# Optimization experiments

Hardware: AMD Instinct MI355X
Metric: run time of the kernel (lower is better)

Reference implementation:

```python
import jax, jax.numpy as jnp
import numpy as np

B, N = 4, 1024
D_MODEL, N_HEADS, D_HEAD, D_COORD = 512, 8, 64, 2


def setup_inputs() -> dict:
    key = jax.random.key(0)
    ks = jax.random.split(key, 8)
    sd = 1.0 / np.sqrt(D_MODEL)
    return {
        "x": jax.random.normal(ks[0], (B, N, D_MODEL), dtype=jnp.float32),
        "positions": jax.random.uniform(ks[1], (N, D_COORD), dtype=jnp.float32) * 32.0,
        "W_Q": jax.random.normal(ks[2], (D_MODEL, N_HEADS * D_HEAD), dtype=jnp.float32) * sd,
        "W_K": jax.random.normal(ks[3], (D_MODEL, N_HEADS * D_HEAD), dtype=jnp.float32) * sd,
        "W_V": jax.random.normal(ks[4], (D_MODEL, N_HEADS * D_HEAD), dtype=jnp.float32) * sd,
        "W_O": jax.random.normal(ks[5], (N_HEADS * D_HEAD, D_MODEL), dtype=jnp.float32) * sd,
        "U": jax.random.normal(ks[6], (N_HEADS, D_HEAD, D_HEAD), dtype=jnp.float32),
        "freqs": jax.random.normal(ks[7], (N_HEADS, D_HEAD // 2, D_COORD), dtype=jnp.float32),
    }


def reference(x, positions, W_Q, W_K, W_V, W_O, U, freqs):
    # x: (B,N,d_model); positions: (N,d_coord); U: (H,dh,dh); freqs: (H,m,d_coord)
    Bn, Nn, _ = x.shape
    H, dh, _ = U.shape
    m = dh // 2
    scale = (dh // 2) ** -0.5

    Q = (x @ W_Q).reshape(Bn, Nn, H, dh)
    K = (x @ W_K).reshape(Bn, Nn, H, dh)
    V = (x @ W_V).reshape(Bn, Nn, H, dh)

    # Active-subspace projector: Pi = qr(U)[0] @ qr(U)[0].T per head
    Uq = jax.vmap(lambda u: jnp.linalg.qr(u)[0])(U)              # (H,dh,dh)
    P = jnp.einsum('hde,hfe->hdf', Uq, Uq)                       # U U^T
    Qp = jnp.einsum('bnhd,hdf->bhnf', Q, P)                      # (B,H,N,dh)
    Kp = jnp.einsum('bnhd,hdf->bhnf', K, P)

    # Relative rotation: R_rel(r_j - r_i) is block-diag 2x2 rotations with
    # angle theta_ijm = freqs_m . (r_j - r_i) = a_jm - a_im (separable), so
    # q^T R(r_j-r_i) k = (R(a_i)q)^T (R(a_j)k)  -- exact RoPE identity.
    ang = jnp.einsum('nc,hmc->hnm', positions, freqs)            # (H,N,m)
    c = jnp.cos(ang)[None]                                       # (1,H,N,m)
    s = jnp.sin(ang)[None]

    def rot(v):  # v: (B,H,N,dh) -> rotated (even, odd) halves (B,H,N,m)
        ve, vo = v[..., ::2], v[..., 1::2]
        return ve * c - vo * s, ve * s + vo * c

    qe, qo = rot(Qp)
    ke, ko = rot(Kp)
    scores = (jnp.einsum('bhim,bhjm->bhij', qe, ke)
              + jnp.einsum('bhim,bhjm->bhij', qo, ko)) * scale   # (B,H,N,N)
    w = jax.nn.softmax(scores, axis=-1)
    out = jnp.einsum('bhij,bjhd->bihd', w, V).reshape(Bn, Nn, H * dh)
    return out @ W_O
```

## Files before the change

### kernel.cpp

```cpp
#include <hip/hip_runtime.h>
#include <math.h>

#define NBATCH 4
#define NSEQ   1024
#define DMODEL 512
#define NH     8
#define DH     64
#define MROWS  (NBATCH*NSEQ)
#define MHALF  (DH/2)

typedef __attribute__((ext_vector_type(8))) short bf16x8;
typedef __attribute__((ext_vector_type(4))) float floatx4;

__device__ __forceinline__ ushort f2bf(float f) {
    union { float f; uint u; } v; v.f = f;
    uint r = v.u + 0x7fffu + ((v.u >> 16) & 1u);
    return (ushort)(r >> 16);
}

__global__ __launch_bounds__(256) void angles_kernel(
    const float* __restrict__ pos, const float* __restrict__ freqs,
    float* __restrict__ cosT, float* __restrict__ sinT)
{
    int idx = blockIdx.x * 256 + threadIdx.x;
    int m = idx & 31;
    int n = (idx >> 5) & 1023;
    int h = idx >> 15;
    float a = pos[n*2+0] * freqs[(h*MHALF+m)*2+0]
            + pos[n*2+1] * freqs[(h*MHALF+m)*2+1];
    cosT[idx] = cosf(a);
    sinT[idx] = sinf(a);
}

__global__ __launch_bounds__(256) void xprep_kernel(
    const float* __restrict__ x, ushort* __restrict__ xb)
{
    int idx = (blockIdx.x * 256 + threadIdx.x) * 8;
    float4 a = *(const float4*)&x[idx];
    float4 b = *(const float4*)&x[idx+4];
    uint4 pk;
    pk.x = (uint)f2bf(a.x) | ((uint)f2bf(a.y) << 16);
    pk.y = (uint)f2bf(a.z) | ((uint)f2bf(a.w) << 16);
    pk.z = (uint)f2bf(b.x) | ((uint)f2bf(b.y) << 16);
    pk.w = (uint)f2bf(b.z) | ((uint)f2bf(b.w) << 16);
    *(uint4*)&xb[idx] = pk;
}

__global__ __launch_bounds__(256) void wprep_kernel(
    const float* __restrict__ Wq, const float* __restrict__ Wk,
    const float* __restrict__ Wv, const float* __restrict__ Wo,
    ushort* __restrict__ Wt)
{
    __shared__ float T[64][65];
    int n0g = blockIdx.x * 64;
    int k0  = blockIdx.y * 64;
    int mat = n0g >> 9;
    const float* W = (mat == 0) ? Wq : ((mat == 1) ? Wk : ((mat == 2) ? Wv : Wo));
    int n0 = n0g & 511;
    int tid = threadIdx.x;
    int c = tid & 63, r = tid >> 6;
    #pragma unroll
    for (int i = 0; i < 16; i++)
        T[r + i*4][c] = W[(k0 + r + i*4) * DMODEL + n0 + c];
    __syncthreads();
    int nl = tid >> 2;
    int kg = tid & 3;
    #pragma unroll
    for (int g = 0; g < 4; g++) {
        int kl = kg * 16 + g * 4;
        uint2 pk;
        pk.x = (uint)f2bf(T[kl+0][nl]) | ((uint)f2bf(T[kl+1][nl]) << 16);
        pk.y = (uint)f2bf(T[kl+2][nl]) | ((uint)f2bf(T[kl+3][nl]) << 16);
        *(uint2*)&Wt[(size_t)(n0g + nl) * DMODEL + k0 + kl] = pk;
    }
}

__global__ __launch_bounds__(256) void qkv_gemm(
    const ushort* __restrict__ xb, const ushort* __restrict__ Wt,
    const float* __restrict__ cosT, const float* __restrict__ sinT,
    ushort* __restrict__ Qb, ushort* __restrict__ Kb, ushort* __restrict__ Vt)
{
    __shared__ ushort As[64 * 40];
    __shared__ ushort Bs[64 * 40];
    __shared__ float  Cs[64][65];

    const int cb = blockIdx.x;
    const int rb = blockIdx.y;
    const int mat = cb >> 3;
    const int c0 = (cb & 7) * 64;
    const int r0 = rb * 64;
    const int ng0 = mat * 512 + c0;

    const int tid = threadIdx.x;
    const int w = tid >> 6, l = tid & 63;
    const int lr = l & 15, lg = l >> 4;

    const int srow = tid >> 2;
    const int sgrp = tid & 3;

    floatx4 acc[4];
    #pragma unroll
    for (int nt = 0; nt < 4; nt++) acc[nt] = (floatx4){0.f,0.f,0.f,0.f};

    for (int k0 = 0; k0 < DMODEL; k0 += 32) {
        __syncthreads();
        *(uint4*)&As[srow*40 + sgrp*8] =
            *(const uint4*)&xb[(size_t)(r0 + srow) * DMODEL + k0 + sgrp*8];
        *(uint4*)&Bs[srow*40 + sgrp*8] =
            *(const uint4*)&Wt[(size_t)(ng0 + srow) * DMODEL + k0 + sgrp*8];
        __syncthreads();

        bf16x8 af = *(const bf16x8*)&As[(16*w + lr)*40 + lg*8];
        #pragma unroll
        for (int nt = 0; nt < 4; nt++) {
            bf16x8 bf = *(const bf16x8*)&Bs[(nt*16 + lr)*40 + lg*8];
            acc[nt] = __builtin_amdgcn_mfma_f32_16x16x32_bf16(af, bf, acc[nt], 0, 0, 0);
        }
    }

    __syncthreads();
    #pragma unroll
    for (int nt = 0; nt < 4; nt++)
        #pragma unroll
        for (int r = 0; r < 4; r++)
            Cs[16*w + lg*4 + r][nt*16 + lr] = acc[nt][r];
    __syncthreads();

    const int tx = tid & 15, ty = tid >> 4;
    const int dbase = (c0 + tx*4) & 63;
    const int h = (mat == 2) ? ((c0 + tx*4) >> 6) + 0 : 0;
    const int head = c0 >> 6;
    (void)h;

    if (mat == 2) {
        int rowbase = r0 + ty * 4;
        int b = rowbase >> 10, n0 = rowbase & 1023;
        size_t vbase = (size_t)(b * NH + head) * DH;
        #pragma unroll
        for (int j = 0; j < 4; j++) {
            ushort us[4];
            #pragma unroll
            for (int i = 0; i < 4; i++) us[i] = f2bf(Cs[ty*4 + i][tx*4 + j]);
            uint2 pk;
            pk.x = (uint)us[0] | ((uint)us[1] << 16);
            pk.y = (uint)us[2] | ((uint)us[3] << 16);
            *(uint2*)&Vt[(vbase + dbase + j) * NSEQ + n0] = pk;
        }
    } else {
        ushort* dst = (mat == 0) ? Qb : Kb;
        #pragma unroll
        for (int i = 0; i < 4; i++) {
            int row = r0 + ty * 4 + i;
            int b = row >> 10, n = row & 1023;
            float v[4];
            #pragma unroll
            for (int p = 0; p < 2; p++) {
                int de = dbase + 2 * p;
                int m = de >> 1;
                float c = cosT[(head * NSEQ + n) * MHALF + m];
                float s = sinT[(head * NSEQ + n) * MHALF + m];
                float ve = Cs[ty*4 + i][tx*4 + 2*p];
                float vo = Cs[ty*4 + i][tx*4 + 2*p + 1];
                v[2*p]     = ve * c - vo * s;
                v[2*p + 1] = ve * s + vo * c;
            }
            uint2 pk;
            pk.x = (uint)f2bf(v[0]) | ((uint)f2bf(v[1]) << 16);
            pk.y = (uint)f2bf(v[2]) | ((uint)f2bf(v[3]) << 16);
            *(uint2*)&dst[((size_t)(b * NH + head) * NSEQ + n) * DH + dbase] = pk;
        }
    }
}

__global__ __launch_bounds__(256) void attn_kernel(
    const ushort* __restrict__ Qb, const ushort* __restrict__ Kb,
    const ushort* __restrict__ Vt, ushort* __restrict__ Obb)
{
    __shared__ ushort Ks[64 * 72];
    __shared__ ushort Vs[64 * 72];
    __shared__ ushort Ps[64 * 72];

    const int tid = threadIdx.x;
    const int w = tid >> 6, l = tid & 63;
    const int lr = l & 15, lg = l >> 4;
    const int bh = blockIdx.y, q0 = blockIdx.x * 64;

    const ushort* Qg = Qb + (size_t)bh * NSEQ * DH;
    const ushort* Kg = Kb + (size_t)bh * NSEQ * DH;
    const ushort* Vg = Vt + (size_t)bh * DH * NSEQ;

    bf16x8 qf[2];
    #pragma unroll
    for (int ks = 0; ks < 2; ks++)
        qf[ks] = *(const bf16x8*)(Qg + (size_t)(q0 + 16*w + lr) * DH + ks*32 + lg*8);

    floatx4 ot[4];
    #pragma unroll
    for (int i = 0; i < 4; i++) ot[i] = (floatx4){0.f, 0.f, 0.f, 0.f};
    float m_run = -INFINITY, l_run = 0.f;
    const float scale = 0.17677669529663687f;

    const int sr = tid >> 2;
    const int sc = (tid & 3) * 16;

    for (int jt = 0; jt < 16; jt++) {
        __syncthreads();
        {
            const ushort* kp = Kg + (size_t)(jt*64 + sr) * DH + sc;
            uint4 ka = *(const uint4*)kp;
            uint4 kb = *(const uint4*)(kp + 8);
            *(uint4*)&Ks[sr*72 + sc]     = ka;
            *(uint4*)&Ks[sr*72 + sc + 8] = kb;
            const ushort* vp = Vg + (size_t)sr * NSEQ + jt*64 + sc;
            uint4 va = *(const uint4*)vp;
            uint4 vb = *(const uint4*)(vp + 8);
            *(uint4*)&Vs[sr*72 + sc]     = va;
            *(uint4*)&Vs[sr*72 + sc + 8] = vb;
        }
        __syncthreads();

        floatx4 st[4];
        #pragma unroll
        for (int jm = 0; jm < 4; jm++) {
            floatx4 acc = (floatx4){0.f, 0.f, 0.f, 0.f};
            #pragma unroll
            for (int ks = 0; ks < 2; ks++) {
                bf16x8 af = *(const bf16x8*)&Ks[(jm*16 + lr)*72 + ks*32 + lg*8];
                acc = __builtin_amdgcn_mfma_f32_16x16x32_bf16(af, qf[ks], acc, 0, 0, 0);
            }
            st[jm] = acc;
        }

        float mx = -INFINITY;
        #pragma unroll
        for (int jm = 0; jm < 4; jm++)
            #pragma unroll
            for (int r = 0; r < 4; r++) {
                st[jm][r] *= scale;
                mx = fmaxf(mx, st[jm][r]);
            }
        mx = fmaxf(mx, __shfl_xor(mx, 16, 64));
        mx = fmaxf(mx, __shfl_xor(mx, 32, 64));
        float mnew = fmaxf(m_run, mx);
        float alpha = __expf(m_run - mnew);
        m_run = mnew;

        float rsum = 0.f;
        #pragma unroll
        for (int jm = 0; jm < 4; jm++) {
            ushort us[4];
            #pragma unroll
            for (int r = 0; r < 4; r++) {
                float p = __expf(st[jm][r] - mnew);
                rsum += p;
                us[r] = f2bf(p);
            }
            uint2 pk;
            pk.x = (uint)us[0] | ((uint)us[1] << 16);
            pk.y = (uint)us[2] | ((uint)us[3] << 16);
            *(uint2*)&Ps[(16*w + lr)*72 + jm*16 + lg*4] = pk;
        }
        rsum += __shfl_xor(rsum, 16, 64);
        rsum += __shfl_xor(rsum, 32, 64);
        l_run = l_run * alpha + rsum;

        #pragma unroll
        for (int dt = 0; dt < 4; dt++)
            #pragma unroll
            for (int r = 0; r < 4; r++)
                ot[dt][r] *= alpha;

        bf16x8 pf[2];
        #pragma unroll
        for (int ks = 0; ks < 2; ks++)
            pf[ks] = *(const bf16x8*)&Ps[(16*w + lr)*72 + ks*32 + lg*8];
        #pragma unroll
        for (int dt = 0; dt < 4; dt++)
            #pragma unroll
            for (int ks = 0; ks < 2; ks++) {
                bf16x8 af = *(const bf16x8*)&Vs[(dt*16 + lr)*72 + ks*32 + lg*8];
                ot[dt] = __builtin_amdgcn_mfma_f32_16x16x32_bf16(af, pf[ks], ot[dt], 0, 0, 0);
            }
    }

    float inv = 1.f / l_run;
    int n = q0 + 16*w + lr;
    #pragma unroll
    for (int dt = 0; dt < 4; dt++) {
        uint2 pk;
        pk.x = (uint)f2bf(ot[dt][0] * inv) | ((uint)f2bf(ot[dt][1] * inv) << 16);
        pk.y = (uint)f2bf(ot[dt][2] * inv) | ((uint)f2bf(ot[dt][3] * inv) << 16);
        *(uint2*)&Obb[((size_t)bh * NSEQ + n) * DH + dt*16 + lg*4] = pk;
    }
}

__global__ __launch_bounds__(256) void out_gemm(
    const ushort* __restrict__ Obb, const ushort* __restrict__ Wt,
    float* __restrict__ out)
{
    __shared__ ushort As[64 * 40];
    __shared__ ushort Bs[64 * 40];
    __shared__ float  Cs[64][65];

    const int cb = blockIdx.x;
    const int rb = blockIdx.y;
    const int c0 = cb * 64, r0 = rb * 64;

    const int tid = threadIdx.x;
    const int w = tid >> 6, l = tid & 63;
    const int lr = l & 15, lg = l >> 4;
    const int srow = tid >> 2;
    const int sgrp = tid & 3;

    const int arow = r0 + srow;
    const int b = arow >> 10, n = arow & 1023;

    floatx4 acc[4];
    #pragma unroll
    for (int nt = 0; nt < 4; nt++) acc[nt] = (floatx4){0.f,0.f,0.f,0.f};

    for (int k0 = 0; k0 < DMODEL; k0 += 32) {
        int h = k0 >> 6;
        int d0 = k0 & 63;
        __syncthreads();
        *(uint4*)&As[srow*40 + sgrp*8] =
            *(const uint4*)&Obb[((size_t)(b * NH + h) * NSEQ + n) * DH + d0 + sgrp*8];
        *(uint4*)&Bs[srow*40 + sgrp*8] =
            *(const uint4*)&Wt[(size_t)(1536 + c0 + srow) * DMODEL + k0 + sgrp*8];
        __syncthreads();

        bf16x8 af = *(const bf16x8*)&As[(16*w + lr)*40 + lg*8];
        #pragma unroll
        for (int nt = 0; nt < 4; nt++) {
            bf16x8 bf = *(const bf16x8*)&Bs[(nt*16 + lr)*40 + lg*8];
            acc[nt] = __builtin_amdgcn_mfma_f32_16x16x32_bf16(af, bf, acc[nt], 0, 0, 0);
        }
    }

    __syncthreads();
    #pragma unroll
    for (int nt = 0; nt < 4; nt++)
        #pragma unroll
        for (int r = 0; r < 4; r++)
            Cs[16*w + lg*4 + r][nt*16 + lr] = acc[nt][r];
    __syncthreads();

    const int tx = tid & 15, ty = tid >> 4;
    #pragma unroll
    for (int i = 0; i < 4; i++) {
        float4 o;
        o.x = Cs[ty*4 + i][tx*4 + 0];
        o.y = Cs[ty*4 + i][tx*4 + 1];
        o.z = Cs[ty*4 + i][tx*4 + 2];
        o.w = Cs[ty*4 + i][tx*4 + 3];
        *(float4*)&out[(size_t)(r0 + ty*4 + i) * DMODEL + c0 + tx*4] = o;
    }
}

extern "C" void kernel_launch(void* const* d_in, const int* in_sizes, int n_in,
                              void* d_out, int out_size, void* d_ws, size_t ws_size,
                              hipStream_t stream) {
    const float* x         = (const float*)d_in[0];
    const float* positions = (const float*)d_in[1];
    const float* Wq        = (const float*)d_in[2];
    const float* Wk        = (const float*)d_in[3];
    const float* Wv        = (const float*)d_in[4];
    const float* Wo        = (const float*)d_in[5];
    const float* freqs     = (const float*)d_in[7];
    float* out = (float*)d_out;

    float*  ws   = (float*)d_ws;
    float*  cosT = ws;
    float*  sinT = cosT + NH*NSEQ*MHALF;
    ushort* xb   = (ushort*)(sinT + NH*NSEQ*MHALF);
    ushort* Wt   = xb + (size_t)MROWS*DMODEL;
    ushort* Qb   = Wt + (size_t)2048*DMODEL;
    ushort* Kb   = Qb + (size_t)NBATCH*NH*NSEQ*DH;
    ushort* Vt   = Kb + (size_t)NBATCH*NH*NSEQ*DH;
    ushort* Obb  = Vt + (size_t)NBATCH*NH*NSEQ*DH;

    angles_kernel<<<dim3(NH*NSEQ*MHALF/256), 256, 0, stream>>>(positions, freqs, cosT, sinT);
    xprep_kernel<<<dim3(MROWS*DMODEL/(256*8)), 256, 0, stream>>>(x, xb);
    wprep_kernel<<<dim3(32, 8), 256, 0, stream>>>(Wq, Wk, Wv, Wo, Wt);
    qkv_gemm<<<dim3(24, 64), 256, 0, stream>>>(xb, Wt, cosT, sinT, Qb, Kb, Vt);
    attn_kernel<<<dim3(16, 32), 256, 0, stream>>>(Qb, Kb, Vt, Obb);
    out_gemm<<<dim3(8, 64), 256, 0, stream>>>(Obb, Wt, out);
}
```

Measured before the change: 139.6 us.

## Split attention over key halves, prefetch K/V tiles, merge prep kernels

Attention now splits the key dimension into two halves (split-K flash attention) so twice as many blocks run, and writes fp32 partial outputs plus running max/sum that a new combine kernel merges. The K/V tile loads are register-prefetched one tile ahead to overlap global loads with MFMA work, and attention gets a launch-bounds occupancy hint. The three prep kernels are fused into one launch to cut launch overhead. In exchange it adds fp32 partial-output traffic and an extra kernel launch for the combine step.

New measurement: 130.7 us. -6.4%, faster.

```diff
diff --git a/kernel.cpp b/kernel.cpp
--- a/kernel.cpp
+++ b/kernel.cpp
@@ -18,60 +18,59 @@
     return (ushort)(r >> 16);
 }
 
-__global__ __launch_bounds__(256) void angles_kernel(
+__global__ __launch_bounds__(256) void prep_kernel(
     const float* __restrict__ pos, const float* __restrict__ freqs,
-    float* __restrict__ cosT, float* __restrict__ sinT)
-{
-    int idx = blockIdx.x * 256 + threadIdx.x;
-    int m = idx & 31;
-    int n = (idx >> 5) & 1023;
-    int h = idx >> 15;
-    float a = pos[n*2+0] * freqs[(h*MHALF+m)*2+0]
-            + pos[n*2+1] * freqs[(h*MHALF+m)*2+1];
-    cosT[idx] = cosf(a);
-    sinT[idx] = sinf(a);
-}
-
-__global__ __launch_bounds__(256) void xprep_kernel(
-    const float* __restrict__ x, ushort* __restrict__ xb)
-{
-    int idx = (blockIdx.x * 256 + threadIdx.x) * 8;
-    float4 a = *(const float4*)&x[idx];
-    float4 b = *(const float4*)&x[idx+4];
-    uint4 pk;
-    pk.x = (uint)f2bf(a.x) | ((uint)f2bf(a.y) << 16);
-    pk.y = (uint)f2bf(a.z) | ((uint)f2bf(a.w) << 16);
-    pk.z = (uint)f2bf(b.x) | ((uint)f2bf(b.y) << 16);
-    pk.w = (uint)f2bf(b.z) | ((uint)f2bf(b.w) << 16);
-    *(uint4*)&xb[idx] = pk;
-}
-
-__global__ __launch_bounds__(256) void wprep_kernel(
+    const float* __restrict__ x,
     const float* __restrict__ Wq, const float* __restrict__ Wk,
     const float* __restrict__ Wv, const float* __restrict__ Wo,
-    ushort* __restrict__ Wt)
+    float* __restrict__ cosT, float* __restrict__ sinT,
+    ushort* __restrict__ xb, ushort* __restrict__ Wt)
 {
     __shared__ float T[64][65];
-    int n0g = blockIdx.x * 64;
-    int k0  = blockIdx.y * 64;
-    int mat = n0g >> 9;
-    const float* W = (mat == 0) ? Wq : ((mat == 1) ? Wk : ((mat == 2) ? Wv : Wo));
-    int n0 = n0g & 511;
-    int tid = threadIdx.x;
-    int c = tid & 63, r = tid >> 6;
-    #pragma unroll
-    for (int i = 0; i < 16; i++)
-        T[r + i*4][c] = W[(k0 + r + i*4) * DMODEL + n0 + c];
-    __syncthreads();
-    int nl = tid >> 2;
-    int kg = tid & 3;
-    #pragma unroll
-    for (int g = 0; g < 4; g++) {
-        int kl = kg * 16 + g * 4;
-        uint2 pk;
-        pk.x = (uint)f2bf(T[kl+0][nl]) | ((uint)f2bf(T[kl+1][nl]) << 16);
-        pk.y = (uint)f2bf(T[kl+2][nl]) | ((uint)f2bf(T[kl+3][nl]) << 16);
-        *(uint2*)&Wt[(size_t)(n0g + nl) * DMODEL + k0 + kl] = pk;
+    const int bid = blockIdx.x;
+    const int tid = threadIdx.x;
+
+    if (bid < 1024) {
+        int idx = bid * 256 + tid;
+        int m = idx & 31;
+        int n = (idx >> 5) & 1023;
+        int h = idx >> 15;
+        float a = pos[n*2+0] * freqs[(h*MHALF+m)*2+0]
+                + pos[n*2+1] * freqs[(h*MHALF+m)*2+1];
+        cosT[idx] = cosf(a);
+        sinT[idx] = sinf(a);
+    } else if (bid < 2048) {
+        int idx = ((bid - 1024) * 256 + tid) * 8;
+        float4 a = *(const float4*)&x[idx];
+        float4 b = *(const float4*)&x[idx+4];
+        uint4 pk;
+        pk.x = (uint)f2bf(a.x) | ((uint)f2bf(a.y) << 16);
+        pk.y = (uint)f2bf(a.z) | ((uint)f2bf(a.w) << 16);
+        pk.z = (uint)f2bf(b.x) | ((uint)f2bf(b.y) << 16);
+        pk.w = (uint)f2bf(b.z) | ((uint)f2bf(b.w) << 16);
+        *(uint4*)&xb[idx] = pk;
+    } else {
+        int b2 = bid - 2048;
+        int n0g = (b2 & 31) * 64;
+        int k0  = (b2 >> 5) * 64;
+        int mat = n0g >> 9;
+        const float* W = (mat == 0) ? Wq : ((mat == 1) ? Wk : ((mat == 2) ? Wv : Wo));
+        int n0 = n0g & 511;
+        int c = tid & 63, r = tid >> 6;
+        #pragma unroll
+        for (int i = 0; i < 16; i++)
+            T[r + i*4][c] = W[(k0 + r + i*4) * DMODEL + n0 + c];
+        __syncthreads();
+        int nl = tid >> 2;
+        int kg = tid & 3;
+        #pragma unroll
+        for (int g = 0; g < 4; g++) {
+            int kl = kg * 16 + g * 4;
+            uint2 pk;
+            pk.x = (uint)f2bf(T[kl+0][nl]) | ((uint)f2bf(T[kl+1][nl]) << 16);
+            pk.y = (uint)f2bf(T[kl+2][nl]) | ((uint)f2bf(T[kl+3][nl]) << 16);
+            *(uint2*)&Wt[(size_t)(n0g + nl) * DMODEL + k0 + kl] = pk;
+        }
     }
 }
 
@@ -127,10 +126,8 @@
     __syncthreads();
 
     const int tx = tid & 15, ty = tid >> 4;
-    const int dbase = (c0 + tx*4) & 63;
-    const int h = (mat == 2) ? ((c0 + tx*4) >> 6) + 0 : 0;
+    const int dbase = tx * 4;
     const int head = c0 >> 6;
-    (void)h;
 
     if (mat == 2) {
         int rowbase = r0 + ty * 4;
@@ -172,9 +169,10 @@
     }
 }
 
-__global__ __launch_bounds__(256) void attn_kernel(
+__global__ __launch_bounds__(256, 4) void attn_kernel(
     const ushort* __restrict__ Qb, const ushort* __restrict__ Kb,
-    const ushort* __restrict__ Vt, ushort* __restrict__ Obb)
+    const ushort* __restrict__ Vt, float* __restrict__ Opart,
+    float2* __restrict__ Ml)
 {
     __shared__ ushort Ks[64 * 72];
     __shared__ ushort Vs[64 * 72];
@@ -184,6 +182,7 @@
     const int w = tid >> 6, l = tid & 63;
     const int lr = l & 15, lg = l >> 4;
     const int bh = blockIdx.y, q0 = blockIdx.x * 64;
+    const int z = blockIdx.z, jt0 = z * 8;
 
     const ushort* Qg = Qb + (size_t)bh * NSEQ * DH;
     const ushort* Kg = Kb + (size_t)bh * NSEQ * DH;
@@ -203,21 +202,29 @@
     const int sr = tid >> 2;
     const int sc = (tid & 3) * 16;
 
-    for (int jt = 0; jt < 16; jt++) {
-        __syncthreads();
-        {
-            const ushort* kp = Kg + (size_t)(jt*64 + sr) * DH + sc;
-            uint4 ka = *(const uint4*)kp;
-            uint4 kb = *(const uint4*)(kp + 8);
-            *(uint4*)&Ks[sr*72 + sc]     = ka;
-            *(uint4*)&Ks[sr*72 + sc + 8] = kb;
-            const ushort* vp = Vg + (size_t)sr * NSEQ + jt*64 + sc;
-            uint4 va = *(const uint4*)vp;
-            uint4 vb = *(const uint4*)(vp + 8);
-            *(uint4*)&Vs[sr*72 + sc]     = va;
-            *(uint4*)&Vs[sr*72 + sc + 8] = vb;
-        }
-        __syncthreads();
+    const ushort* kp = Kg + (size_t)(jt0*64 + sr) * DH + sc;
+    uint4 ka  = *(const uint4*)kp;
+    uint4 kb2 = *(const uint4*)(kp + 8);
+    const ushort* vp = Vg + (size_t)sr * NSEQ + jt0*64 + sc;
+    uint4 va  = *(const uint4*)vp;
+    uint4 vb2 = *(const uint4*)(vp + 8);
+
+    for (int jt = jt0; jt < jt0 + 8; jt++) {
+        __syncthreads();
+        *(uint4*)&Ks[sr*72 + sc]     = ka;
+        *(uint4*)&Ks[sr*72 + sc + 8] = kb2;
+        *(uint4*)&Vs[sr*72 + sc]     = va;
+        *(uint4*)&Vs[sr*72 + sc + 8] = vb2;
+        __syncthreads();
+
+        if (jt < jt0 + 7) {
+            const ushort* kn = Kg + (size_t)((jt+1)*64 + sr) * DH + sc;
+            ka  = *(const uint4*)kn;
+            kb2 = *(const uint4*)(kn + 8);
+            const ushort* vn = Vg + (size_t)sr * NSEQ + (jt+1)*64 + sc;
+            va  = *(const uint4*)vn;
+            vb2 = *(const uint4*)(vn + 8);
+        }
 
         floatx4 st[4];
         #pragma unroll
@@ -283,14 +290,38 @@
             }
     }
 
-    float inv = 1.f / l_run;
     int n = q0 + 16*w + lr;
-    #pragma unroll
-    for (int dt = 0; dt < 4; dt++) {
+    size_t obase = ((size_t)(z * 32 + bh) * NSEQ + n) * DH;
+    #pragma unroll
+    for (int dt = 0; dt < 4; dt++)
+        *(floatx4*)&Opart[obase + dt*16 + lg*4] = ot[dt];
+    if (lg == 0)
+        Ml[(size_t)(z * 32 + bh) * NSEQ + n] = make_float2(m_run, l_run);
+}
+
+__global__ __launch_bounds__(256) void combine_kernel(
+    const float* __restrict__ Op, const float2* __restrict__ Ml,
+    ushort* __restrict__ Obb)
+{
+    int idx = blockIdx.x * 256 + threadIdx.x;
+    int qi = idx >> 2;
+    int dp = (idx & 3) << 4;
+    float2 a = Ml[qi], b = Ml[32768 + qi];
+    float m = fmaxf(a.x, b.x);
+    float w1 = __expf(a.x - m), w2 = __expf(b.x - m);
+    float inv = 1.f / (a.y * w1 + b.y * w2);
+    w1 *= inv; w2 *= inv;
+    const float* p1 = Op + (size_t)qi * 64 + dp;
+    const float* p2 = p1 + (size_t)32768 * 64;
+    ushort* po = Obb + (size_t)qi * 64 + dp;
+    #pragma unroll
+    for (int g = 0; g < 4; g++) {
+        float4 u = *(const float4*)(p1 + g*4);
+        float4 v = *(const float4*)(p2 + g*4);
         uint2 pk;
-        pk.x = (uint)f2bf(ot[dt][0] * inv) | ((uint)f2bf(ot[dt][1] * inv) << 16);
-        pk.y = (uint)f2bf(ot[dt][2] * inv) | ((uint)f2bf(ot[dt][3] * inv) << 16);
-        *(uint2*)&Obb[((size_t)bh * NSEQ + n) * DH + dt*16 + lg*4] = pk;
+        pk.x = (uint)f2bf(u.x*w1 + v.x*w2) | ((uint)f2bf(u.y*w1 + v.y*w2) << 16);
+        pk.y = (uint)f2bf(u.z*w1 + v.z*w2) | ((uint)f2bf(u.w*w1 + v.w*w2) << 16);
+        *(uint2*)(po + g*4) = pk;
     }
 }
 
@@ -369,20 +400,22 @@
     const float* freqs     = (const float*)d_in[7];
     float* out = (float*)d_out;
 
-    float*  ws   = (float*)d_ws;
-    float*  cosT = ws;
-    float*  sinT = cosT + NH*NSEQ*MHALF;
-    ushort* xb   = (ushort*)(sinT + NH*NSEQ*MHALF);
-    ushort* Wt   = xb + (size_t)MROWS*DMODEL;
-    ushort* Qb   = Wt + (size_t)2048*DMODEL;
-    ushort* Kb   = Qb + (size_t)NBATCH*NH*NSEQ*DH;
-    ushort* Vt   = Kb + (size_t)NBATCH*NH*NSEQ*DH;
-    ushort* Obb  = Vt + (size_t)NBATCH*NH*NSEQ*DH;
-
-    angles_kernel<<<dim3(NH*NSEQ*MHALF/256), 256, 0, stream>>>(positions, freqs, cosT, sinT);
-    xprep_kernel<<<dim3(MROWS*DMODEL/(256*8)), 256, 0, stream>>>(x, xb);
-    wprep_kernel<<<dim3(32, 8), 256, 0, stream>>>(Wq, Wk, Wv, Wo, Wt);
+    float*  ws    = (float*)d_ws;
+    float*  cosT  = ws;
+    float*  sinT  = cosT + NH*NSEQ*MHALF;
+    float*  Opart = sinT + NH*NSEQ*MHALF;
+    float2* Ml    = (float2*)(Opart + 2*(size_t)NBATCH*NH*NSEQ*DH);
+    ushort* xb    = (ushort*)(Ml + 2*(size_t)NBATCH*NH*NSEQ);
+    ushort* Wt    = xb + (size_t)MROWS*DMODEL;
+    ushort* Qb    = Wt + (size_t)2048*DMODEL;
+    ushort* Kb    = Qb + (size_t)NBATCH*NH*NSEQ*DH;
+    ushort* Vt    = Kb + (size_t)NBATCH*NH*NSEQ*DH;
+    ushort* Obb   = Vt + (size_t)NBATCH*NH*NSEQ*DH;
+
+    prep_kernel<<<dim3(2304), 256, 0, stream>>>(positions, freqs, x, Wq, Wk, Wv, Wo,
+                                                cosT, sinT, xb, Wt);
     qkv_gemm<<<dim3(24, 64), 256, 0, stream>>>(xb, Wt, cosT, sinT, Qb, Kb, Vt);
-    attn_kernel<<<dim3(16, 32), 256, 0, stream>>>(Qb, Kb, Vt, Obb);
+    attn_kernel<<<dim3(16, 32, 2), 256, 0, stream>>>(Qb, Kb, Vt, Opart, Ml);
+    combine_kernel<<<dim3(512), 256, 0, stream>>>(Opart, Ml, Obb);
     out_gemm<<<dim3(8, 64), 256, 0, stream>>>(Obb, Wt, out);
 }
```
